# Performance work log

Hardware: AMD Instinct MI355X
Metric: run time of the kernel (lower is better)

The kernel has to match this reference:

```python
import jax, jax.numpy as jnp
import numpy as np

DIM = 1024
CTX_DIM = 1024
HEADS = 16
HEAD_DIM = DIM // HEADS


def setup_inputs() -> dict:
    key = jax.random.key(0)
    ks = jax.random.split(key, 6)
    B, N, M = 4, 2048, 2048
    s = 0.02
    return {
        "x": jax.random.normal(ks[0], (B, N, DIM), dtype=jnp.float32),
        "context": jax.random.normal(ks[1], (B, M, CTX_DIM), dtype=jnp.float32),
        "Wq": jax.random.normal(ks[2], (DIM, DIM), dtype=jnp.float32) * s,
        "Wk": jax.random.normal(ks[3], (CTX_DIM, DIM), dtype=jnp.float32) * s,
        "Wv": jax.random.normal(ks[4], (CTX_DIM, DIM), dtype=jnp.float32) * s,
        "Wo": jax.random.normal(ks[5], (DIM, DIM), dtype=jnp.float32) * s,
        "bo": jnp.zeros((DIM,), dtype=jnp.float32),
    }


def reference(x, context, Wq, Wk, Wv, Wo, bo):
    B, N, C = x.shape
    scale = HEAD_DIM ** -0.5
    # projections then split heads: (B, H, N, Dh)
    q = (x @ Wq.T).reshape(B, N, HEADS, HEAD_DIM).transpose(0, 2, 1, 3)
    k = (context @ Wk.T).reshape(B, -1, HEADS, HEAD_DIM).transpose(0, 2, 1, 3)
    v = (context @ Wv.T).reshape(B, -1, HEADS, HEAD_DIM).transpose(0, 2, 1, 3)
    attn = jnp.einsum('bhnd,bhmd->bhnm', q, k) * scale
    attn = jax.nn.softmax(attn, axis=-1)
    out = jnp.einsum('bhnm,bhmd->bhnd', attn, v)
    out = out.transpose(0, 2, 1, 3).reshape(B, N, C)
    return out @ Wo.T + bo
```

## Files before the change

### kernel.cpp

```cpp
#include <hip/hip_runtime.h>
#include <hip/hip_bf16.h>
#include <stdint.h>

typedef __bf16 bf16x8 __attribute__((ext_vector_type(8)));
typedef float  f32x4  __attribute__((ext_vector_type(4)));

#define SEQ   2048
#define DIMV  1024
#define HEADS 16
#define HDIM  64
#define KD    1024

#define SCL 0.1803368801111204f
#define THRRAW 44.36f

static __device__ __forceinline__ unsigned short f2bf(float f) {
  union { float f; unsigned u; } v; v.f = f;
  unsigned r = (v.u + 0x7fffu + ((v.u >> 16) & 1u)) >> 16;
  return (unsigned short)r;
}

static __device__ __forceinline__ unsigned cvtpk(float a, float b) {
  unsigned r;
  asm("v_cvt_pk_bf16_f32 %0, %1, %2" : "=v"(r) : "v"(a), "v"(b));
  return r;
}

__global__ void cvt_kernel(const float* __restrict__ src,
                           ushort4* __restrict__ dst, int n4) {
  int i = blockIdx.x * 256 + threadIdx.x;
  if (i >= n4) return;
  float4 v = reinterpret_cast<const float4*>(src)[i];
  ushort4 o;
  o.x = f2bf(v.x); o.y = f2bf(v.y); o.z = f2bf(v.z); o.w = f2bf(v.w);
  dst[i] = o;
}

static __device__ __forceinline__ void gload_lds16(const unsigned short* g,
                                                   unsigned short* l) {
  __builtin_amdgcn_global_load_lds(
      (const __attribute__((address_space(1))) unsigned int*)g,
      (__attribute__((address_space(3))) unsigned int*)l, 16, 0, 0);
}

template <int MODE>
__global__ __launch_bounds__(256) void gemm_bt(
    const unsigned short* __restrict__ A,
    const unsigned short* __restrict__ B,
    void* __restrict__ Cv,
    const float* __restrict__ bias) {
  __shared__ unsigned short As[128 * 32];
  __shared__ unsigned short Bs[128 * 32];
  const int t = threadIdx.x;
  const int lane = t & 63, wave = t >> 6;
  const int fr = lane & 15, fq = lane >> 4;
  const int m0 = blockIdx.x * 128, n0 = blockIdx.y * 128;
  const int wm0 = (wave >> 1) * 64, wn0 = (wave & 1) * 64;

  const int srow = wave * 16 + (lane >> 2);
  const int scol = (lane & 3) * 8;
  const unsigned short* gA = A + (size_t)(m0 + srow) * KD + scol;
  const unsigned short* gB = B + (size_t)(n0 + srow) * KD + scol;
  unsigned short* lA = &As[srow * 32 + scol];
  unsigned short* lB = &Bs[srow * 32 + scol];

  f32x4 acc[4][4];
#pragma unroll
  for (int i = 0; i < 4; ++i)
#pragma unroll
    for (int j = 0; j < 4; ++j) acc[i][j] = (f32x4){0.f, 0.f, 0.f, 0.f};

  for (int k0 = 0;;) {
    gload_lds16(gA + k0, lA);
    gload_lds16(gA + (size_t)64 * KD + k0, lA + 64 * 32);
    gload_lds16(gB + k0, lB);
    gload_lds16(gB + (size_t)64 * KD + k0, lB + 64 * 32);
    __syncthreads();

    bf16x8 af[4], bfv[4];
#pragma unroll
    for (int mi = 0; mi < 4; ++mi)
      af[mi] = *(const bf16x8*)&As[(wm0 + mi * 16 + fr) * 32 + fq * 8];
#pragma unroll
    for (int nj = 0; nj < 4; ++nj)
      bfv[nj] = *(const bf16x8*)&Bs[(wn0 + nj * 16 + fr) * 32 + fq * 8];
#pragma unroll
    for (int mi = 0; mi < 4; ++mi)
#pragma unroll
      for (int nj = 0; nj < 4; ++nj)
        acc[mi][nj] = __builtin_amdgcn_mfma_f32_16x16x32_bf16(
            af[mi], bfv[nj], acc[mi][nj], 0, 0, 0);

    k0 += 32;
    if (k0 >= KD) break;
    __syncthreads();
  }

#pragma unroll
  for (int mi = 0; mi < 4; ++mi)
#pragma unroll
    for (int nj = 0; nj < 4; ++nj)
#pragma unroll
      for (int r = 0; r < 4; ++r) {
        const int gr = m0 + wm0 + mi * 16 + fq * 4 + r;
        const int gc = n0 + wn0 + nj * 16 + fr;
        const float v = acc[mi][nj][r];
        if (MODE == 0) {
          size_t off = (((size_t)(gr >> 11) * HEADS + (gc >> 6)) * SEQ +
                        (gr & 2047)) * HDIM + (gc & 63);
          ((unsigned short*)Cv)[off] = f2bf(v);
        } else if (MODE == 1) {
          size_t off = (size_t)(gc >> 11) * (DIMV * SEQ) + (size_t)gr * SEQ +
                       (gc & 2047);
          ((unsigned short*)Cv)[off] = f2bf(v);
        } else {
          ((float*)Cv)[(size_t)gr * DIMV + gc] = v + bias[gc];
        }
      }
}

__global__ __launch_bounds__(256, 3) void attn_kernel(
    const unsigned short* __restrict__ q, const unsigned short* __restrict__ k,
    const unsigned short* __restrict__ vt, unsigned short* __restrict__ ao) {
  __shared__ unsigned short Pl[4][32 * 64];
  const int t = threadIdx.x, lane = t & 63, wave = t >> 6;
  const int fr = lane & 15, fq = lane >> 4;
  const int bh = blockIdx.y;
  const int b = bh >> 4, h = bh & 15;
  const int qrow0 = blockIdx.x * 128 + wave * 32;

  const unsigned short* qp = q + ((size_t)bh * SEQ + qrow0) * HDIM;
  const unsigned short* kp = k + (size_t)bh * SEQ * HDIM;
  const unsigned short* vp = vt + (size_t)b * (DIMV * SEQ) + (size_t)(h * HDIM) * SEQ;
  char* plw = (char*)&Pl[wave][0];

  bf16x8 qf[2][2];
#pragma unroll
  for (int mi = 0; mi < 2; ++mi)
#pragma unroll
    for (int kc = 0; kc < 2; ++kc)
      qf[mi][kc] = *(const bf16x8*)(qp + (size_t)(mi * 16 + fr) * HDIM + kc * 32 + fq * 8);

  f32x4 oacc[2][4];
  float m_s[2], lrow[2];
#pragma unroll
  for (int mi = 0; mi < 2; ++mi) {
#pragma unroll
    for (int dj = 0; dj < 4; ++dj) oacc[mi][dj] = (f32x4){0.f, 0.f, 0.f, 0.f};
    m_s[mi] = -1e30f; lrow[mi] = 0.f;
  }

  for (int kb = 0; kb < SEQ; kb += 64) {
    bf16x8 kf[4][2], vf[4][2];
#pragma unroll
    for (int nj = 0; nj < 4; ++nj)
#pragma unroll
      for (int kc = 0; kc < 2; ++kc)
        kf[nj][kc] = *(const bf16x8*)(kp + (size_t)(kb + nj * 16 + fr) * HDIM + kc * 32 + fq * 8);
#pragma unroll
    for (int dj = 0; dj < 4; ++dj)
#pragma unroll
      for (int kc = 0; kc < 2; ++kc)
        vf[dj][kc] = *(const bf16x8*)(vp + (size_t)(dj * 16 + fr) * SEQ + kb + kc * 32 + fq * 8);

    f32x4 sacc[2][4];
#pragma unroll
    for (int mi = 0; mi < 2; ++mi)
#pragma unroll
      for (int nj = 0; nj < 4; ++nj) sacc[mi][nj] = (f32x4){0.f, 0.f, 0.f, 0.f};
    __builtin_amdgcn_s_setprio(1);
#pragma unroll
    for (int mi = 0; mi < 2; ++mi)
#pragma unroll
      for (int nj = 0; nj < 4; ++nj)
#pragma unroll
        for (int kc = 0; kc < 2; ++kc)
          sacc[mi][nj] = __builtin_amdgcn_mfma_f32_16x16x32_bf16(
              kf[nj][kc], qf[mi][kc], sacc[mi][nj], 0, 0, 0);
    __builtin_amdgcn_s_setprio(0);

#pragma unroll
    for (int mi = 0; mi < 2; ++mi) {
      float t0 = fmaxf(fmaxf(sacc[mi][0][0], sacc[mi][0][1]),
                       fmaxf(sacc[mi][0][2], sacc[mi][0][3]));
      float t1 = fmaxf(fmaxf(sacc[mi][1][0], sacc[mi][1][1]),
                       fmaxf(sacc[mi][1][2], sacc[mi][1][3]));
      float t2 = fmaxf(fmaxf(sacc[mi][2][0], sacc[mi][2][1]),
                       fmaxf(sacc[mi][2][2], sacc[mi][2][3]));
      float t3 = fmaxf(fmaxf(sacc[mi][3][0], sacc[mi][3][1]),
                       fmaxf(sacc[mi][3][2], sacc[mi][3][3]));
      float tmax = fmaxf(fmaxf(t0, t1), fmaxf(t2, t3));
      tmax = fmaxf(tmax, __shfl_xor(tmax, 16));
      tmax = fmaxf(tmax, __shfl_xor(tmax, 32));

      if (__any(tmax > m_s[mi] + THRRAW)) {
        const float mnew = fmaxf(m_s[mi], tmax);
        const float fo = exp2f((m_s[mi] - mnew) * SCL);
        m_s[mi] = mnew;
        lrow[mi] *= fo;
#pragma unroll
        for (int dj = 0; dj < 4; ++dj)
#pragma unroll
          for (int r = 0; r < 4; ++r) oacc[mi][dj][r] *= fo;
      }

      const float nm = m_s[mi] * SCL;
      const int row = mi * 16 + fr;
      float lacc = 0.f;
#pragma unroll
      for (int nj = 0; nj < 4; ++nj) {
        float p0 = exp2f(__builtin_fmaf(sacc[mi][nj][0], SCL, -nm));
        float p1 = exp2f(__builtin_fmaf(sacc[mi][nj][1], SCL, -nm));
        float p2 = exp2f(__builtin_fmaf(sacc[mi][nj][2], SCL, -nm));
        float p3 = exp2f(__builtin_fmaf(sacc[mi][nj][3], SCL, -nm));
        lacc += (p0 + p1) + (p2 + p3);
        unsigned w0 = cvtpk(p0, p1);
        unsigned w1 = cvtpk(p2, p3);
        const int colb = (nj * 16 + fq * 4) * 2;
        *(uint2*)(plw + ((row * 128 + colb) ^ ((row & 7) << 4))) =
            make_uint2(w0, w1);
      }
      lrow[mi] += lacc;
    }

    bf16x8 pf[2][2];
#pragma unroll
    for (int mi = 0; mi < 2; ++mi)
#pragma unroll
      for (int kc = 0; kc < 2; ++kc) {
        const int row = mi * 16 + fr, colb = (kc * 32 + fq * 8) * 2;
        pf[mi][kc] = *(const bf16x8*)(plw + ((row * 128 + colb) ^ ((row & 7) << 4)));
      }
    __builtin_amdgcn_s_setprio(1);
#pragma unroll
    for (int mi = 0; mi < 2; ++mi)
#pragma unroll
      for (int dj = 0; dj < 4; ++dj)
#pragma unroll
        for (int kc = 0; kc < 2; ++kc)
          oacc[mi][dj] = __builtin_amdgcn_mfma_f32_16x16x32_bf16(
              vf[dj][kc], pf[mi][kc], oacc[mi][dj], 0, 0, 0);
    __builtin_amdgcn_s_setprio(0);
  }

#pragma unroll
  for (int mi = 0; mi < 2; ++mi) {
    float lt = lrow[mi];
    lt += __shfl_xor(lt, 16);
    lt += __shfl_xor(lt, 32);
    const float inv = 1.f / lt;
    const size_t grow = (size_t)b * SEQ + blockIdx.x * 128 + wave * 32 + mi * 16 + fr;
#pragma unroll
    for (int dj = 0; dj < 4; ++dj) {
      unsigned w0 = cvtpk(oacc[mi][dj][0] * inv, oacc[mi][dj][1] * inv);
      unsigned w1 = cvtpk(oacc[mi][dj][2] * inv, oacc[mi][dj][3] * inv);
      const int col = h * HDIM + dj * 16 + fq * 4;
      *(uint2*)&ao[grow * DIMV + col] = make_uint2(w0, w1);
    }
  }
}

extern "C" void kernel_launch(void* const* d_in, const int* in_sizes, int n_in,
                              void* d_out, int out_size, void* d_ws, size_t ws_size,
                              hipStream_t stream) {
  const float* x   = (const float*)d_in[0];
  const float* ctx = (const float*)d_in[1];
  const float* Wq  = (const float*)d_in[2];
  const float* Wk  = (const float*)d_in[3];
  const float* Wv  = (const float*)d_in[4];
  const float* Wo  = (const float*)d_in[5];
  const float* bo  = (const float*)d_in[6];

  char* ws = (char*)d_ws;
  unsigned short* xb  = (unsigned short*)(ws);
  unsigned short* cb  = (unsigned short*)(ws + 16777216);
  unsigned short* wqb = (unsigned short*)(ws + 33554432);
  unsigned short* wkb = (unsigned short*)(ws + 35651584);
  unsigned short* wvb = (unsigned short*)(ws + 37748736);
  unsigned short* wob = (unsigned short*)(ws + 39845888);
  unsigned short* qb  = (unsigned short*)(ws + 41943040);
  unsigned short* kb  = (unsigned short*)(ws + 58720256);
  unsigned short* vtb = (unsigned short*)(ws + 75497472);

  auto cvt = [&](const float* s, unsigned short* d, int n) {
    int n4 = n >> 2;
    cvt_kernel<<<(n4 + 255) / 256, 256, 0, stream>>>(s, (ushort4*)d, n4);
  };
  const int NTOK = 4 * SEQ;
  cvt(x,   xb,  NTOK * DIMV);
  cvt(ctx, cb,  NTOK * DIMV);
  cvt(Wq,  wqb, DIMV * DIMV);
  cvt(Wk,  wkb, DIMV * DIMV);
  cvt(Wv,  wvb, DIMV * DIMV);
  cvt(Wo,  wob, DIMV * DIMV);

  gemm_bt<0><<<dim3(64, 8), 256, 0, stream>>>(xb, wqb, qb, nullptr);
  gemm_bt<0><<<dim3(64, 8), 256, 0, stream>>>(cb, wkb, kb, nullptr);
  gemm_bt<1><<<dim3(8, 64), 256, 0, stream>>>(wvb, cb, vtb, nullptr);

  unsigned short* aob = xb;
  attn_kernel<<<dim3(16, 64), 256, 0, stream>>>(qb, kb, vtb, aob);

  gemm_bt<2><<<dim3(64, 8), 256, 0, stream>>>(aob, wob, (float*)d_out, bo);
}
```

Before: 475.7 us.

## Stage K tiles in double-buffered LDS, shrink attention tiles, and remap blocks by XCD

The attention kernel now loads K tiles into LDS with direct global-to-LDS copies, double-buffered so the next tile is prefetched while the current one is used. Each wave handles 16 query rows instead of 32, giving 64 rows per block, 2048 blocks and a higher occupancy target. A 1D grid is remapped so blocks of the same batch-head land on the same XCD, which should improve L2 reuse of K and V. The cost is a block-wide barrier on every iteration and only half the K/V reuse per wave, since each block now covers fewer query rows.

```diff
diff --git a/kernel.cpp b/kernel.cpp
--- a/kernel.cpp
+++ b/kernel.cpp
@@ -119,144 +119,142 @@
       }
 }
 
-__global__ __launch_bounds__(256, 3) void attn_kernel(
+__global__ __launch_bounds__(256, 4) void attn_kernel(
     const unsigned short* __restrict__ q, const unsigned short* __restrict__ k,
     const unsigned short* __restrict__ vt, unsigned short* __restrict__ ao) {
-  __shared__ unsigned short Pl[4][32 * 64];
+  __shared__ unsigned short Ks[2][64 * 64];
+  __shared__ unsigned short Pl[4][16 * 64];
   const int t = threadIdx.x, lane = t & 63, wave = t >> 6;
   const int fr = lane & 15, fq = lane >> 4;
-  const int bh = blockIdx.y;
+  const int wg = blockIdx.x;
+  const int xcd = wg & 7, idx = wg >> 3;
+  const int bh = (xcd << 3) | (idx >> 5);
+  const int qt = idx & 31;
   const int b = bh >> 4, h = bh & 15;
-  const int qrow0 = blockIdx.x * 128 + wave * 32;
+  const int qrow0 = qt * 64 + wave * 16;
 
   const unsigned short* qp = q + ((size_t)bh * SEQ + qrow0) * HDIM;
   const unsigned short* kp = k + (size_t)bh * SEQ * HDIM;
   const unsigned short* vp = vt + (size_t)b * (DIMV * SEQ) + (size_t)(h * HDIM) * SEQ;
   char* plw = (char*)&Pl[wave][0];
 
-  bf16x8 qf[2][2];
-#pragma unroll
-  for (int mi = 0; mi < 2; ++mi)
-#pragma unroll
-    for (int kc = 0; kc < 2; ++kc)
-      qf[mi][kc] = *(const bf16x8*)(qp + (size_t)(mi * 16 + fr) * HDIM + kc * 32 + fq * 8);
-
-  f32x4 oacc[2][4];
-  float m_s[2], lrow[2];
-#pragma unroll
-  for (int mi = 0; mi < 2; ++mi) {
-#pragma unroll
-    for (int dj = 0; dj < 4; ++dj) oacc[mi][dj] = (f32x4){0.f, 0.f, 0.f, 0.f};
-    m_s[mi] = -1e30f; lrow[mi] = 0.f;
+  const int rb = t >> 3;
+  const int cb = (t & 7) << 4;
+
+  bf16x8 qf[2];
+#pragma unroll
+  for (int kc = 0; kc < 2; ++kc)
+    qf[kc] = *(const bf16x8*)(qp + (size_t)fr * HDIM + kc * 32 + fq * 8);
+
+  f32x4 oacc[4];
+#pragma unroll
+  for (int dj = 0; dj < 4; ++dj) oacc[dj] = (f32x4){0.f, 0.f, 0.f, 0.f};
+  float m_s = -1e30f, lrow = 0.f;
+
+#pragma unroll
+  for (int i = 0; i < 2; ++i) {
+    const int r = rb + i * 32;
+    gload_lds16(kp + (size_t)r * HDIM + ((cb ^ ((r & 7) << 4)) >> 1),
+                (unsigned short*)((char*)&Ks[0][0] + i * 4096 + t * 16));
   }
-
-  for (int kb = 0; kb < SEQ; kb += 64) {
-    bf16x8 kf[4][2], vf[4][2];
-#pragma unroll
-    for (int nj = 0; nj < 4; ++nj)
-#pragma unroll
-      for (int kc = 0; kc < 2; ++kc)
-        kf[nj][kc] = *(const bf16x8*)(kp + (size_t)(kb + nj * 16 + fr) * HDIM + kc * 32 + fq * 8);
+  __syncthreads();
+
+  int cur = 0;
+  for (int kb = 0; kb < SEQ; kb += 64, cur ^= 1) {
+    if (kb + 64 < SEQ) {
+#pragma unroll
+      for (int i = 0; i < 2; ++i) {
+        const int r = rb + i * 32;
+        gload_lds16(kp + (size_t)(kb + 64 + r) * HDIM + ((cb ^ ((r & 7) << 4)) >> 1),
+                    (unsigned short*)((char*)&Ks[cur ^ 1][0] + i * 4096 + t * 16));
+      }
+    }
+    bf16x8 vf[4][2];
 #pragma unroll
     for (int dj = 0; dj < 4; ++dj)
 #pragma unroll
       for (int kc = 0; kc < 2; ++kc)
         vf[dj][kc] = *(const bf16x8*)(vp + (size_t)(dj * 16 + fr) * SEQ + kb + kc * 32 + fq * 8);
 
-    f32x4 sacc[2][4];
-#pragma unroll
-    for (int mi = 0; mi < 2; ++mi)
-#pragma unroll
-      for (int nj = 0; nj < 4; ++nj) sacc[mi][nj] = (f32x4){0.f, 0.f, 0.f, 0.f};
-    __builtin_amdgcn_s_setprio(1);
-#pragma unroll
-    for (int mi = 0; mi < 2; ++mi)
+    const char* kls = (const char*)&Ks[cur][0];
+    f32x4 sacc[4];
+#pragma unroll
+    for (int nj = 0; nj < 4; ++nj) sacc[nj] = (f32x4){0.f, 0.f, 0.f, 0.f};
+#pragma unroll
+    for (int kc = 0; kc < 2; ++kc) {
+      bf16x8 kf[4];
 #pragma unroll
       for (int nj = 0; nj < 4; ++nj)
-#pragma unroll
-        for (int kc = 0; kc < 2; ++kc)
-          sacc[mi][nj] = __builtin_amdgcn_mfma_f32_16x16x32_bf16(
-              kf[nj][kc], qf[mi][kc], sacc[mi][nj], 0, 0, 0);
-    __builtin_amdgcn_s_setprio(0);
-
-#pragma unroll
-    for (int mi = 0; mi < 2; ++mi) {
-      float t0 = fmaxf(fmaxf(sacc[mi][0][0], sacc[mi][0][1]),
-                       fmaxf(sacc[mi][0][2], sacc[mi][0][3]));
-      float t1 = fmaxf(fmaxf(sacc[mi][1][0], sacc[mi][1][1]),
-                       fmaxf(sacc[mi][1][2], sacc[mi][1][3]));
-      float t2 = fmaxf(fmaxf(sacc[mi][2][0], sacc[mi][2][1]),
-                       fmaxf(sacc[mi][2][2], sacc[mi][2][3]));
-      float t3 = fmaxf(fmaxf(sacc[mi][3][0], sacc[mi][3][1]),
-                       fmaxf(sacc[mi][3][2], sacc[mi][3][3]));
-      float tmax = fmaxf(fmaxf(t0, t1), fmaxf(t2, t3));
-      tmax = fmaxf(tmax, __shfl_xor(tmax, 16));
-      tmax = fmaxf(tmax, __shfl_xor(tmax, 32));
-
-      if (__any(tmax > m_s[mi] + THRRAW)) {
-        const float mnew = fmaxf(m_s[mi], tmax);
-        const float fo = exp2f((m_s[mi] - mnew) * SCL);
-        m_s[mi] = mnew;
-        lrow[mi] *= fo;
-#pragma unroll
-        for (int dj = 0; dj < 4; ++dj)
-#pragma unroll
-          for (int r = 0; r < 4; ++r) oacc[mi][dj][r] *= fo;
-      }
-
-      const float nm = m_s[mi] * SCL;
-      const int row = mi * 16 + fr;
-      float lacc = 0.f;
-#pragma unroll
-      for (int nj = 0; nj < 4; ++nj) {
-        float p0 = exp2f(__builtin_fmaf(sacc[mi][nj][0], SCL, -nm));
-        float p1 = exp2f(__builtin_fmaf(sacc[mi][nj][1], SCL, -nm));
-        float p2 = exp2f(__builtin_fmaf(sacc[mi][nj][2], SCL, -nm));
-        float p3 = exp2f(__builtin_fmaf(sacc[mi][nj][3], SCL, -nm));
-        lacc += (p0 + p1) + (p2 + p3);
-        unsigned w0 = cvtpk(p0, p1);
-        unsigned w1 = cvtpk(p2, p3);
-        const int colb = (nj * 16 + fq * 4) * 2;
-        *(uint2*)(plw + ((row * 128 + colb) ^ ((row & 7) << 4))) =
-            make_uint2(w0, w1);
-      }
-      lrow[mi] += lacc;
-    }
-
-    bf16x8 pf[2][2];
-#pragma unroll
-    for (int mi = 0; mi < 2; ++mi)
-#pragma unroll
-      for (int kc = 0; kc < 2; ++kc) {
-        const int row = mi * 16 + fr, colb = (kc * 32 + fq * 8) * 2;
-        pf[mi][kc] = *(const bf16x8*)(plw + ((row * 128 + colb) ^ ((row & 7) << 4)));
-      }
-    __builtin_amdgcn_s_setprio(1);
-#pragma unroll
-    for (int mi = 0; mi < 2; ++mi)
+        kf[nj] = *(const bf16x8*)(kls + (nj * 16 + fr) * 128 +
+                                  ((kc * 64 + fq * 16) ^ ((fr & 7) << 4)));
+      __builtin_amdgcn_s_setprio(1);
+#pragma unroll
+      for (int nj = 0; nj < 4; ++nj)
+        sacc[nj] = __builtin_amdgcn_mfma_f32_16x16x32_bf16(
+            kf[nj], qf[kc], sacc[nj], 0, 0, 0);
+      __builtin_amdgcn_s_setprio(0);
+    }
+
+    float t0 = fmaxf(fmaxf(sacc[0][0], sacc[0][1]), fmaxf(sacc[0][2], sacc[0][3]));
+    float t1 = fmaxf(fmaxf(sacc[1][0], sacc[1][1]), fmaxf(sacc[1][2], sacc[1][3]));
+    float t2 = fmaxf(fmaxf(sacc[2][0], sacc[2][1]), fmaxf(sacc[2][2], sacc[2][3]));
+    float t3 = fmaxf(fmaxf(sacc[3][0], sacc[3][1]), fmaxf(sacc[3][2], sacc[3][3]));
+    float tmax = fmaxf(fmaxf(t0, t1), fmaxf(t2, t3));
+    tmax = fmaxf(tmax, __shfl_xor(tmax, 16));
+    tmax = fmaxf(tmax, __shfl_xor(tmax, 32));
+
+    if (__any(tmax > m_s + THRRAW)) {
+      const float mnew = fmaxf(m_s, tmax);
+      const float fo = exp2f((m_s - mnew) * SCL);
+      m_s = mnew;
+      lrow *= fo;
 #pragma unroll
       for (int dj = 0; dj < 4; ++dj)
 #pragma unroll
-        for (int kc = 0; kc < 2; ++kc)
-          oacc[mi][dj] = __builtin_amdgcn_mfma_f32_16x16x32_bf16(
-              vf[dj][kc], pf[mi][kc], oacc[mi][dj], 0, 0, 0);
-    __builtin_amdgcn_s_setprio(0);
+        for (int r = 0; r < 4; ++r) oacc[dj][r] *= fo;
+    }
+
+    const float nm = m_s * SCL;
+    float lacc = 0.f;
+#pragma unroll
+    for (int nj = 0; nj < 4; ++nj) {
+      float p0 = exp2f(__builtin_fmaf(sacc[nj][0], SCL, -nm));
+      float p1 = exp2f(__builtin_fmaf(sacc[nj][1], SCL, -nm));
+      float p2 = exp2f(__builtin_fmaf(sacc[nj][2], SCL, -nm));
+      float p3 = exp2f(__builtin_fmaf(sacc[nj][3], SCL, -nm));
+      lacc += (p0 + p1) + (p2 + p3);
+      unsigned w0 = cvtpk(p0, p1);
+      unsigned w1 = cvtpk(p2, p3);
+      const int colb = (nj * 16 + fq * 4) * 2;
+      *(uint2*)(plw + ((fr * 128 + colb) ^ ((fr & 7) << 4))) = make_uint2(w0, w1);
+    }
+    lrow += lacc;
+
+#pragma unroll
+    for (int kc = 0; kc < 2; ++kc) {
+      bf16x8 pf = *(const bf16x8*)(plw + ((fr * 128 + kc * 64 + fq * 16) ^ ((fr & 7) << 4)));
+      __builtin_amdgcn_s_setprio(1);
+#pragma unroll
+      for (int dj = 0; dj < 4; ++dj)
+        oacc[dj] = __builtin_amdgcn_mfma_f32_16x16x32_bf16(
+            vf[dj][kc], pf, oacc[dj], 0, 0, 0);
+      __builtin_amdgcn_s_setprio(0);
+    }
+
+    __syncthreads();
   }
 
-#pragma unroll
-  for (int mi = 0; mi < 2; ++mi) {
-    float lt = lrow[mi];
-    lt += __shfl_xor(lt, 16);
-    lt += __shfl_xor(lt, 32);
-    const float inv = 1.f / lt;
-    const size_t grow = (size_t)b * SEQ + blockIdx.x * 128 + wave * 32 + mi * 16 + fr;
-#pragma unroll
-    for (int dj = 0; dj < 4; ++dj) {
-      unsigned w0 = cvtpk(oacc[mi][dj][0] * inv, oacc[mi][dj][1] * inv);
-      unsigned w1 = cvtpk(oacc[mi][dj][2] * inv, oacc[mi][dj][3] * inv);
-      const int col = h * HDIM + dj * 16 + fq * 4;
-      *(uint2*)&ao[grow * DIMV + col] = make_uint2(w0, w1);
-    }
+  float lt = lrow;
+  lt += __shfl_xor(lt, 16);
+  lt += __shfl_xor(lt, 32);
+  const float inv = 1.f / lt;
+  const size_t grow = (size_t)b * SEQ + qt * 64 + wave * 16 + fr;
+#pragma unroll
+  for (int dj = 0; dj < 4; ++dj) {
+    unsigned w0 = cvtpk(oacc[dj][0] * inv, oacc[dj][1] * inv);
+    unsigned w1 = cvtpk(oacc[dj][2] * inv, oacc[dj][3] * inv);
+    const int col = h * HDIM + dj * 16 + fq * 4;
+    *(uint2*)&ao[grow * DIMV + col] = make_uint2(w0, w1);
   }
 }
 
@@ -299,7 +297,7 @@
   gemm_bt<1><<<dim3(8, 64), 256, 0, stream>>>(wvb, cb, vtb, nullptr);
 
   unsigned short* aob = xb;
-  attn_kernel<<<dim3(16, 64), 256, 0, stream>>>(qb, kb, vtb, aob);
+  attn_kernel<<<dim3(2048), 256, 0, stream>>>(qb, kb, vtb, aob);
 
   gemm_bt<2><<<dim3(64, 8), 256, 0, stream>>>(aob, wob, (float*)d_out, bo);
 }
```

Result: slower. 498.4 us (+4.8%).
